# Kernel tuning notes

Measured on AMD Instinct MI355X. Metric: run time of the kernel, lower is better.

## Reference

```python
import jax, jax.numpy as jnp
import numpy as np

B, MAX_LAYERS = 512, 64
UNITS = 4 * MAX_LAYERS  # 256; also the sequence length after expand_dims


def setup_inputs() -> dict:
    key = jax.random.key(0)
    k1, k2, k3 = jax.random.split(key, 3)
    x = jax.random.normal(k1, (B, UNITS), dtype=jnp.float32)
    # scale weights ~ Glorot so gates don't saturate
    kernel = jax.random.normal(k2, (1, 8 * UNITS), dtype=jnp.float32) * 0.5
    recurrent_kernel = jax.random.normal(k3, (UNITS, 8 * UNITS), dtype=jnp.float32) * (1.0 / np.sqrt(UNITS))
    return {"x": x, "kernel": kernel, "recurrent_kernel": recurrent_kernel}


def _nas_step(c, h, x_t, kernel, rec_kernel):
    # x_t: [B, 1]; c, h: [B, U]
    inp = x_t @ kernel        # [B, 8U]
    m = h @ rec_kernel        # [B, 8U]
    i = jnp.split(inp, 8, axis=1)
    mm = jnp.split(m, 8, axis=1)
    sig, tanh, relu = jax.nn.sigmoid, jnp.tanh, jax.nn.relu
    # first layer (NASCell fixed wiring)
    l1_0 = sig(i[0] + mm[0]);  l1_1 = relu(i[1] + mm[1])
    l1_2 = sig(i[2] + mm[2]);  l1_3 = relu(i[3] * mm[3])
    l1_4 = tanh(i[4] + mm[4]); l1_5 = sig(i[5] + mm[5])
    l1_6 = tanh(i[6] + mm[6]); l1_7 = sig(i[7] + mm[7])
    # second layer
    l2_0 = tanh(l1_0 * l1_1); l2_1 = tanh(l1_2 + l1_3)
    l2_2 = tanh(l1_4 * l1_5); l2_3 = sig(l1_6 + l1_7)
    # inject the cell state
    l2_0 = tanh(l2_0 + c)
    # third layer
    new_c = l2_0 * l2_1
    l3_1 = tanh(l2_2 + l2_3)
    # final layer
    new_h = tanh(new_c * l3_1)
    return new_c, new_h


def reference(x, kernel, recurrent_kernel):
    # call(): inputs = expand_dims(inputs, -1) -> [B, T, 1], T = 4*max_layers
    xs = jnp.swapaxes(x[..., None], 0, 1)  # [T, B, 1]
    bsz = x.shape[0]
    units = recurrent_kernel.shape[0]
    c0 = jnp.zeros((bsz, units), x.dtype)
    h0 = jnp.zeros((bsz, units), x.dtype)

    def step(carry, x_t):
        c, h = carry
        c, h = _nas_step(c, h, x_t, kernel, recurrent_kernel)
        return (c, h), None

    (c, h), _ = jax.lax.scan(step, (c0, h0), xs)
    return h  # keras RNN(return_sequences=False): last output [B, U]
```

## Files before the change

### kernel.cpp

```cpp
#include <hip/hip_runtime.h>


#define NRB     16
#define RB_ROWS 32
#define WU      16
#define NSLOT   4
#define SLAB_BYTES (RB_ROWS*256*2)
#define SLOT_BYTES (NRB*SLAB_BYTES)
#define SPIN_STEP 500000
#define SPIN_RDV  5000000

typedef _Float16 f16;
typedef f16  f16x8 __attribute__((ext_vector_type(8)));
typedef float f32x4 __attribute__((ext_vector_type(4)));
typedef unsigned int u32;
typedef unsigned long long u64;

__device__ __forceinline__ float sigm_(float xx) {
  float e = __expf(-xx);
  return __builtin_amdgcn_rcpf(1.0f + e);
}
__device__ __forceinline__ float tanh_(float xx) {
  float ax = __builtin_fabsf(xx);
  float e  = __expf(-2.0f * ax);
  float r  = (1.0f - e) * __builtin_amdgcn_rcpf(1.0f + e);
  return __builtin_copysignf(r, xx);
}

__device__ __forceinline__ u32 rmw_add0_l2(u32* p) {
  u32 r, z = 0;
  asm volatile("global_atomic_add %0, %1, %2, off sc0\n\ts_waitcnt vmcnt(0)"
               : "=v"(r) : "v"(p), "v"(z) : "memory");
  return r;
}
__device__ __forceinline__ void inc_l2(u32* p, u32 v) {
  asm volatile("global_atomic_add %0, %1, off" :: "v"(p), "v"(v) : "memory");
}

__device__ __forceinline__ void gld_lds16(const void* g, void* l) {
  __builtin_amdgcn_global_load_lds(
      (const __attribute__((address_space(1))) unsigned int*)g,
      (__attribute__((address_space(3))) unsigned int*)l, 16, 0, 0);
}

__global__ __launch_bounds__(256, 1)
void nas_cell_rnn(const float* __restrict__ x,
                  const float* __restrict__ kern,
                  const float* __restrict__ rec,
                  float* __restrict__ out,
                  u32* __restrict__ ws32,
                  char* __restrict__ hbuf)
{
  const int tid  = threadIdx.x;
  const int lane = tid & 63;
  const int ww   = tid >> 6;
  const int wg   = blockIdx.x;
  const int rb   = wg & 15;
  const int w    = wg >> 4;

  __shared__ f16   h_lds[RB_ROWS][256];
  __shared__ float m_T[128][36];
  __shared__ float x_lds[RB_ROWS][256];
  __shared__ u32   fast_s;

  const int l15 = lane & 15;
  const int lg4 = lane >> 4;

  u32* const pcnt = ws32 + 288 + rb*32;

  u32 xcc;
  asm("s_getreg_b32 %0, hwreg(HW_REG_XCC_ID)" : "=s"(xcc));
  u32 base = 0;
  if (tid == 0) {
    __hip_atomic_store(&ws32[wg], xcc, __ATOMIC_RELAXED, __HIP_MEMORY_SCOPE_AGENT);
    __hip_atomic_fetch_add(&ws32[256], 1u, __ATOMIC_RELEASE, __HIP_MEMORY_SCOPE_AGENT);
    int sp = 0;
    while (__hip_atomic_load(&ws32[256], __ATOMIC_RELAXED, __HIP_MEMORY_SCOPE_AGENT) < 256u)
      if (++sp > SPIN_RDV) break;
    u32 ok = 1;
    for (int w2 = 0; w2 < 16; ++w2) {
      u32 o = __hip_atomic_load(&ws32[w2*16 + rb], __ATOMIC_RELAXED, __HIP_MEMORY_SCOPE_AGENT);
      ok &= (o == xcc) ? 1u : 0u;
    }
    fast_s = ok;
    base = ok ? rmw_add0_l2(pcnt)
              : __hip_atomic_load(pcnt, __ATOMIC_RELAXED, __HIP_MEMORY_SCOPE_AGENT);
    __hip_atomic_fetch_add(&ws32[260], 1u, __ATOMIC_RELEASE, __HIP_MEMORY_SCOPE_AGENT);
    sp = 0;
    while (__hip_atomic_load(&ws32[260], __ATOMIC_RELAXED, __HIP_MEMORY_SCOPE_AGENT) < 256u)
      if (++sp > SPIN_RDV) break;
  }
  __syncthreads();
  const bool fast = (fast_s != 0);

  f16x8 bfr[2][2][8];
#pragma unroll
  for (int ci = 0; ci < 2; ++ci) {
    const int colidx = 32*ww + 16*ci + l15;
    const int gate   = colidx >> 4;
    const int ucol   = colidx & 15;
    const int gcol   = gate*256 + w*WU + ucol;
#pragma unroll
    for (int sb = 0; sb < 8; ++sb) {
      f16x8 vh, vl;
#pragma unroll
      for (int e = 0; e < 8; ++e) {
        const int k = 32*sb + 8*lg4 + e;
        const float r = rec[k*2048 + gcol];
        const f16 hi = (f16)r;
        vh[e] = hi;
        vl[e] = (f16)(r - (float)hi);
      }
      bfr[ci][0][sb] = vh;
      bfr[ci][1][sb] = vl;
    }
  }

  {
    const float4* src = (const float4*)(x + (size_t)rb*RB_ROWS*256);
    float4* dst = (float4*)&x_lds[0][0];
#pragma unroll
    for (int i = 0; i < 8; ++i) dst[tid + 256*i] = src[tid + 256*i];
  }

  const int ul = tid & 15;
  const int b0 = tid >> 4;
  float kv[8];
#pragma unroll
  for (int g = 0; g < 8; ++g) kv[g] = kern[g*256 + w*WU + ul];

  float cst0 = 0.0f, cst1 = 0.0f;
  int sr = 0, sw = 1;

  char* const hrb = hbuf + (size_t)rb * SLAB_BYTES;

  for (int t = 0; t < 256; ++t) {
    if (t > 0) {
      if (tid == 0) {
        const u32 tgt = base + 16u * (u32)t;
        int sp = 0;
        if (fast) {
          while (rmw_add0_l2(pcnt) < tgt)
            if (++sp > SPIN_STEP) break;
        } else {
          while (__hip_atomic_load(pcnt, __ATOMIC_RELAXED,
                                   __HIP_MEMORY_SCOPE_AGENT) < tgt)
            if (++sp > SPIN_STEP) break;
        }
      }
      __syncthreads();

      const char* srcb = hrb + (size_t)sr * SLOT_BYTES;
      if (fast) {
#pragma unroll
        for (int i = 0; i < 4; ++i) {
          const int off = ww*4096 + i*1024;
          gld_lds16(srcb + off + lane*16, (char*)&h_lds[0][0] + off);
        }
        asm volatile("s_waitcnt vmcnt(0)" ::: "memory");
      } else {
        const u64* p = (const u64*)(srcb + (size_t)tid * 64);
        u64 v[8];
#pragma unroll
        for (int j = 0; j < 8; ++j)
          v[j] = __hip_atomic_load(p + j, __ATOMIC_RELAXED, __HIP_MEMORY_SCOPE_AGENT);
        u64* lp = (u64*)((char*)&h_lds[0][0] + (size_t)tid * 64);
#pragma unroll
        for (int j = 0; j < 8; ++j) lp[j] = v[j];
      }
    }
    __syncthreads();

    if (t > 0) {
      f32x4 acc00 = {0,0,0,0}, acc01 = {0,0,0,0}, acc10 = {0,0,0,0}, acc11 = {0,0,0,0};
      const f16* hb = &h_lds[0][0] + l15*256;
      const int axor = (l15 & 7) << 3;
#pragma unroll
      for (int sb = 0; sb < 8; ++sb) {
        const int col = (32*sb + 8*lg4) ^ axor;
        const f16x8 a0 = *(const f16x8*)(hb + col);
        const f16x8 a1 = *(const f16x8*)(hb + 16*256 + col);
        acc00 = __builtin_amdgcn_mfma_f32_16x16x32_f16(a0, bfr[0][0][sb], acc00, 0, 0, 0);
        acc10 = __builtin_amdgcn_mfma_f32_16x16x32_f16(a1, bfr[0][0][sb], acc10, 0, 0, 0);
        acc01 = __builtin_amdgcn_mfma_f32_16x16x32_f16(a0, bfr[1][0][sb], acc01, 0, 0, 0);
        acc11 = __builtin_amdgcn_mfma_f32_16x16x32_f16(a1, bfr[1][0][sb], acc11, 0, 0, 0);
        acc00 = __builtin_amdgcn_mfma_f32_16x16x32_f16(a0, bfr[0][1][sb], acc00, 0, 0, 0);
        acc10 = __builtin_amdgcn_mfma_f32_16x16x32_f16(a1, bfr[0][1][sb], acc10, 0, 0, 0);
        acc01 = __builtin_amdgcn_mfma_f32_16x16x32_f16(a0, bfr[1][1][sb], acc01, 0, 0, 0);
        acc11 = __builtin_amdgcn_mfma_f32_16x16x32_f16(a1, bfr[1][1][sb], acc11, 0, 0, 0);
      }
      const int mc0 = 32*ww + l15;
      const int r0  = 4*lg4;
      *(f32x4*)&m_T[mc0     ][r0]      = acc00;
      *(f32x4*)&m_T[mc0     ][16 + r0] = acc10;
      *(f32x4*)&m_T[mc0 + 16][r0]      = acc01;
      *(f32x4*)&m_T[mc0 + 16][16 + r0] = acc11;
    }
    __syncthreads();

#pragma unroll
    for (int cell = 0; cell < 2; ++cell) {
      const int   b  = b0 + 16*cell;
      const float xv = x_lds[b][t];
      const float cc = cell ? cst1 : cst0;
      float mg[8];
#pragma unroll
      for (int g = 0; g < 8; ++g)
        mg[g] = (t == 0) ? 0.0f : m_T[g*WU + ul][b];

      const float i0 = xv*kv[0], i1 = xv*kv[1], i2 = xv*kv[2], i3 = xv*kv[3];
      const float i4 = xv*kv[4], i5 = xv*kv[5], i6 = xv*kv[6], i7 = xv*kv[7];

      const float l1_0 = sigm_(i0 + mg[0]);
      const float l1_1 = fmaxf(i1 + mg[1], 0.0f);
      const float l1_2 = sigm_(i2 + mg[2]);
      const float l1_3 = fmaxf(i3 * mg[3], 0.0f);
      const float l1_4 = tanh_(i4 + mg[4]);
      const float l1_5 = sigm_(i5 + mg[5]);
      const float l1_6 = tanh_(i6 + mg[6]);
      const float l1_7 = sigm_(i7 + mg[7]);

      float       l2_0 = tanh_(l1_0 * l1_1);
      const float l2_1 = tanh_(l1_2 + l1_3);
      const float l2_2 = tanh_(l1_4 * l1_5);
      const float l2_3 = sigm_(l1_6 + l1_7);

      l2_0 = tanh_(l2_0 + cc);
      const float nc = l2_0 * l2_1;
      const float l3 = tanh_(l2_2 + l2_3);
      const float nh = tanh_(nc * l3);
      if (cell) cst1 = nc; else cst0 = nc;

      if (t == 255) {
        out[(rb*RB_ROWS + b)*256 + w*WU + ul] = nh;
      } else {
        const int idx = (b*256 + (w*WU + ul)) ^ ((b & 7) << 3);
        f16* dst = (f16*)(hrb + (size_t)sw * SLOT_BYTES) + idx;
        if (fast) {
          *dst = (f16)nh;
        } else {
          unsigned short us = __builtin_bit_cast(unsigned short, (f16)nh);
          __hip_atomic_store((unsigned short*)dst, us,
                             __ATOMIC_RELAXED, __HIP_MEMORY_SCOPE_AGENT);
        }
      }
    }
    __syncthreads();

    if (t < 255 && tid == 0) {
      if (fast) inc_l2(pcnt, 1u);
      else __hip_atomic_fetch_add(pcnt, 1u, __ATOMIC_RELAXED, __HIP_MEMORY_SCOPE_AGENT);
    }
    sr = sw; sw = (sw == NSLOT-1) ? 0 : sw + 1;
  }
}

extern "C" void kernel_launch(void* const* d_in, const int* in_sizes, int n_in,
                              void* d_out, int out_size, void* d_ws, size_t ws_size,
                              hipStream_t stream) {
  (void)in_sizes; (void)n_in; (void)out_size; (void)ws_size;
  const float* x    = (const float*)d_in[0];
  const float* kern = (const float*)d_in[1];
  const float* rec  = (const float*)d_in[2];
  float* out = (float*)d_out;

  u32*  ws32 = (u32*)d_ws;
  char* hbuf = (char*)d_ws + 4096;

  hipMemsetAsync(d_ws, 0, 4096, stream);
  hipLaunchKernelGGL(nas_cell_rnn, dim3(256), dim3(256), 0, stream,
                     x, kern, rec, out, ws32, hbuf);
}
```

Before: 716.4 us.

## Double threads per block and load h tiles directly into MFMA registers

Block size goes from 256 to 512 threads. Each wave now handles one 16-row half of the batch tile, so each thread computes a single cell instead of two. The per-step staging of h into LDS is removed: waves read their A fragments straight from global memory into registers. That drops one LDS round trip and one barrier per step, and the swizzle on stores is dropped. It adds a vmcnt wait before the step barrier and lowers the spin limit, at the cost of more VGPR pressure per thread and uncoalesced 16-byte global reads.

```diff
diff --git a/kernel.cpp b/kernel.cpp
--- a/kernel.cpp
+++ b/kernel.cpp
@@ -7,7 +7,7 @@
 #define NSLOT   4
 #define SLAB_BYTES (RB_ROWS*256*2)
 #define SLOT_BYTES (NRB*SLAB_BYTES)
-#define SPIN_STEP 500000
+#define SPIN_STEP 100000
 #define SPIN_RDV  5000000
 
 typedef _Float16 f16;
@@ -37,13 +37,7 @@
   asm volatile("global_atomic_add %0, %1, off" :: "v"(p), "v"(v) : "memory");
 }
 
-__device__ __forceinline__ void gld_lds16(const void* g, void* l) {
-  __builtin_amdgcn_global_load_lds(
-      (const __attribute__((address_space(1))) unsigned int*)g,
-      (__attribute__((address_space(3))) unsigned int*)l, 16, 0, 0);
-}
-
-__global__ __launch_bounds__(256, 1)
+__global__ __launch_bounds__(512, 2)
 void nas_cell_rnn(const float* __restrict__ x,
                   const float* __restrict__ kern,
                   const float* __restrict__ rec,
@@ -53,13 +47,14 @@
 {
   const int tid  = threadIdx.x;
   const int lane = tid & 63;
-  const int ww   = tid >> 6;
+  const int wv   = tid >> 6;
+  const int rh   = wv >> 2;
+  const int cg   = wv & 3;
   const int wg   = blockIdx.x;
   const int rb   = wg & 15;
   const int w    = wg >> 4;
 
-  __shared__ f16   h_lds[RB_ROWS][256];
-  __shared__ float m_T[128][36];
+  __shared__ float m_T[128][40];
   __shared__ float x_lds[RB_ROWS][256];
   __shared__ u32   fast_s;
 
@@ -96,7 +91,7 @@
   f16x8 bfr[2][2][8];
 #pragma unroll
   for (int ci = 0; ci < 2; ++ci) {
-    const int colidx = 32*ww + 16*ci + l15;
+    const int colidx = cg*32 + ci*16 + l15;
     const int gate   = colidx >> 4;
     const int ucol   = colidx & 15;
     const int gcol   = gate*256 + w*WU + ucol;
@@ -120,16 +115,16 @@
     const float4* src = (const float4*)(x + (size_t)rb*RB_ROWS*256);
     float4* dst = (float4*)&x_lds[0][0];
 #pragma unroll
-    for (int i = 0; i < 8; ++i) dst[tid + 256*i] = src[tid + 256*i];
+    for (int i = 0; i < 4; ++i) dst[tid + 512*i] = src[tid + 512*i];
   }
 
   const int ul = tid & 15;
-  const int b0 = tid >> 4;
+  const int b  = tid >> 4;
   float kv[8];
 #pragma unroll
   for (int g = 0; g < 8; ++g) kv[g] = kern[g*256 + w*WU + ul];
 
-  float cst0 = 0.0f, cst1 = 0.0f;
+  float cst = 0.0f;
   int sr = 0, sw = 1;
 
   char* const hrb = hbuf + (size_t)rb * SLAB_BYTES;
@@ -149,60 +144,41 @@
         }
       }
       __syncthreads();
-
-      const char* srcb = hrb + (size_t)sr * SLOT_BYTES;
+      __builtin_amdgcn_sched_barrier(0);
+
+      const char* arow = hrb + (size_t)sr * SLOT_BYTES + (size_t)(rh*16 + l15) * 512
+                       + lg4*16;
+      f16x8 a[8];
       if (fast) {
 #pragma unroll
-        for (int i = 0; i < 4; ++i) {
-          const int off = ww*4096 + i*1024;
-          gld_lds16(srcb + off + lane*16, (char*)&h_lds[0][0] + off);
+        for (int sb = 0; sb < 8; ++sb)
+          a[sb] = *(const f16x8*)(arow + sb*64);
+      } else {
+#pragma unroll
+        for (int sb = 0; sb < 8; ++sb) {
+          const u64* p = (const u64*)(arow + sb*64);
+          const u64 lo = __hip_atomic_load(p,     __ATOMIC_RELAXED, __HIP_MEMORY_SCOPE_AGENT);
+          const u64 hi = __hip_atomic_load(p + 1, __ATOMIC_RELAXED, __HIP_MEMORY_SCOPE_AGENT);
+          union { u64 q[2]; f16x8 v; } u2; u2.q[0] = lo; u2.q[1] = hi;
+          a[sb] = u2.v;
         }
-        asm volatile("s_waitcnt vmcnt(0)" ::: "memory");
-      } else {
-        const u64* p = (const u64*)(srcb + (size_t)tid * 64);
-        u64 v[8];
-#pragma unroll
-        for (int j = 0; j < 8; ++j)
-          v[j] = __hip_atomic_load(p + j, __ATOMIC_RELAXED, __HIP_MEMORY_SCOPE_AGENT);
-        u64* lp = (u64*)((char*)&h_lds[0][0] + (size_t)tid * 64);
-#pragma unroll
-        for (int j = 0; j < 8; ++j) lp[j] = v[j];
-      }
+      }
+
+      f32x4 acc0 = {0,0,0,0}, acc1 = {0,0,0,0};
+#pragma unroll
+      for (int sb = 0; sb < 8; ++sb) {
+        acc0 = __builtin_amdgcn_mfma_f32_16x16x32_f16(a[sb], bfr[0][0][sb], acc0, 0, 0, 0);
+        acc1 = __builtin_amdgcn_mfma_f32_16x16x32_f16(a[sb], bfr[1][0][sb], acc1, 0, 0, 0);
+        acc0 = __builtin_amdgcn_mfma_f32_16x16x32_f16(a[sb], bfr[0][1][sb], acc0, 0, 0, 0);
+        acc1 = __builtin_amdgcn_mfma_f32_16x16x32_f16(a[sb], bfr[1][1][sb], acc1, 0, 0, 0);
+      }
+      *(f32x4*)&m_T[cg*32      + l15][rh*16 + 4*lg4] = acc0;
+      *(f32x4*)&m_T[cg*32 + 16 + l15][rh*16 + 4*lg4] = acc1;
     }
     __syncthreads();
 
-    if (t > 0) {
-      f32x4 acc00 = {0,0,0,0}, acc01 = {0,0,0,0}, acc10 = {0,0,0,0}, acc11 = {0,0,0,0};
-      const f16* hb = &h_lds[0][0] + l15*256;
-      const int axor = (l15 & 7) << 3;
-#pragma unroll
-      for (int sb = 0; sb < 8; ++sb) {
-        const int col = (32*sb + 8*lg4) ^ axor;
-        const f16x8 a0 = *(const f16x8*)(hb + col);
-        const f16x8 a1 = *(const f16x8*)(hb + 16*256 + col);
-        acc00 = __builtin_amdgcn_mfma_f32_16x16x32_f16(a0, bfr[0][0][sb], acc00, 0, 0, 0);
-        acc10 = __builtin_amdgcn_mfma_f32_16x16x32_f16(a1, bfr[0][0][sb], acc10, 0, 0, 0);
-        acc01 = __builtin_amdgcn_mfma_f32_16x16x32_f16(a0, bfr[1][0][sb], acc01, 0, 0, 0);
-        acc11 = __builtin_amdgcn_mfma_f32_16x16x32_f16(a1, bfr[1][0][sb], acc11, 0, 0, 0);
-        acc00 = __builtin_amdgcn_mfma_f32_16x16x32_f16(a0, bfr[0][1][sb], acc00, 0, 0, 0);
-        acc10 = __builtin_amdgcn_mfma_f32_16x16x32_f16(a1, bfr[0][1][sb], acc10, 0, 0, 0);
-        acc01 = __builtin_amdgcn_mfma_f32_16x16x32_f16(a0, bfr[1][1][sb], acc01, 0, 0, 0);
-        acc11 = __builtin_amdgcn_mfma_f32_16x16x32_f16(a1, bfr[1][1][sb], acc11, 0, 0, 0);
-      }
-      const int mc0 = 32*ww + l15;
-      const int r0  = 4*lg4;
-      *(f32x4*)&m_T[mc0     ][r0]      = acc00;
-      *(f32x4*)&m_T[mc0     ][16 + r0] = acc10;
-      *(f32x4*)&m_T[mc0 + 16][r0]      = acc01;
-      *(f32x4*)&m_T[mc0 + 16][16 + r0] = acc11;
-    }
-    __syncthreads();
-
-#pragma unroll
-    for (int cell = 0; cell < 2; ++cell) {
-      const int   b  = b0 + 16*cell;
+    {
       const float xv = x_lds[b][t];
-      const float cc = cell ? cst1 : cst0;
       float mg[8];
 #pragma unroll
       for (int g = 0; g < 8; ++g)
@@ -225,17 +201,16 @@
       const float l2_2 = tanh_(l1_4 * l1_5);
       const float l2_3 = sigm_(l1_6 + l1_7);
 
-      l2_0 = tanh_(l2_0 + cc);
+      l2_0 = tanh_(l2_0 + cst);
       const float nc = l2_0 * l2_1;
       const float l3 = tanh_(l2_2 + l2_3);
       const float nh = tanh_(nc * l3);
-      if (cell) cst1 = nc; else cst0 = nc;
+      cst = nc;
 
       if (t == 255) {
         out[(rb*RB_ROWS + b)*256 + w*WU + ul] = nh;
       } else {
-        const int idx = (b*256 + (w*WU + ul)) ^ ((b & 7) << 3);
-        f16* dst = (f16*)(hrb + (size_t)sw * SLOT_BYTES) + idx;
+        f16* dst = (f16*)(hrb + (size_t)sw * SLOT_BYTES) + (b*256 + w*WU + ul);
         if (fast) {
           *dst = (f16)nh;
         } else {
@@ -245,6 +220,7 @@
         }
       }
     }
+    asm volatile("s_waitcnt vmcnt(0)" ::: "memory");
     __syncthreads();
 
     if (t < 255 && tid == 0) {
@@ -268,6 +244,6 @@
   char* hbuf = (char*)d_ws + 4096;
 
   hipMemsetAsync(d_ws, 0, 4096, stream);
-  hipLaunchKernelGGL(nas_cell_rnn, dim3(256), dim3(256), 0, stream,
+  hipLaunchKernelGGL(nas_cell_rnn, dim3(256), dim3(512), 0, stream,
                      x, kern, rec, out, ws32, hbuf);
 }
```

Result: slower. 954.2 us (+33.2%).
